# Performance work log

Measured on AMD Instinct MI355X. Metric: run time of the kernel, lower is better.

Reference implementation:

```python
import jax, jax.numpy as jnp
import numpy as np

B, D, H, Wd = 8, 64, 256, 256
EMB = 256
NFEAT = 18
NBINS = 16


def setup_inputs() -> dict:
    key = jax.random.key(0)
    k1, k2 = jax.random.split(key, 2)
    volume = jax.random.normal(k1, (B, D, H, Wd), jnp.float32)
    W = jax.random.normal(k2, (NFEAT, EMB), jnp.float32) * 0.1
    b = jnp.zeros((EMB,), jnp.float32)
    gamma = jnp.ones((EMB,), jnp.float32)
    beta = jnp.zeros((EMB,), jnp.float32)
    return {"volume": volume, "W": W, "b": b, "gamma": gamma, "beta": beta}


def _slice_features(sl):
    # sl: [H, W] single slice; mask derived from 80th percentile threshold
    h, w = sl.shape
    flat = sl.reshape(-1)
    npix = flat.shape[0]
    thresh = jnp.quantile(flat, 0.8)  # torch.quantile default: linear interp
    mask = flat >= thresh
    mf = mask.astype(sl.dtype)
    n = mf.sum()  # >= 1 by construction (max always passes)

    mean = (mf * flat).sum() / n
    c = flat - mean
    std = jnp.sqrt((mf * c * c).sum() / n)  # unbiased=False
    std_eps = jnp.maximum(std, 1e-6)
    skew = jnp.clip(((mf * c**3).sum() / n) / std_eps**3, -50.0, 50.0)
    kurt = jnp.clip(((mf * c**4).sum() / n) / std_eps**4, 0.0, 100.0)
    msq = (mf * flat * flat).sum() / n
    absmean = (mf * jnp.abs(flat)).sum() / n

    # sorted masked values: unmasked pushed to +inf end
    big = jnp.finfo(sl.dtype).max
    vs = jnp.sort(jnp.where(mask, flat, big))
    nm1 = n - 1.0
    last = nm1.astype(jnp.int32)

    def quant(p):
        pos = p * nm1
        lo = jnp.floor(pos)
        fr = pos - lo
        lo_i = lo.astype(jnp.int32)
        hi_i = jnp.minimum(lo_i + 1, last)
        return vs[lo_i] * (1.0 - fr) + vs[hi_i] * fr

    q25, q50, q75 = quant(0.25), quant(0.5), quant(0.75)
    vmin = vs[0]
    vmax = vs[last]

    # 16-bin histogram entropy over masked values (torch.histc semantics)
    rng = vmax - vmin
    denom = jnp.where(rng > 0, rng, 1.0)
    bins = jnp.clip(jnp.floor((flat - vmin) / denom * NBINS).astype(jnp.int32), 0, NBINS - 1)
    hist = jnp.zeros((NBINS,), sl.dtype).at[bins].add(mf)
    probs = jnp.maximum(hist / jnp.maximum(hist.sum(), 1.0), 1e-6)
    ent = jnp.where(jnp.isclose(vmin, vmax), 0.0, -(probs * jnp.log(probs)).sum())

    # numpy-style gradient magnitude (central diff interior, one-sided edges)
    gy, gx = jnp.gradient(sl)
    gm = jnp.sqrt(gy * gy + gx * gx).reshape(-1)
    gm_mean = (mf * gm).sum() / n
    gm_std = jnp.sqrt((mf * (gm - gm_mean) ** 2).sum() / n)

    # normalized centroid of the mask
    yi = (jnp.arange(npix) // w).astype(sl.dtype)
    xi = (jnp.arange(npix) % w).astype(sl.dtype)
    cy = (mf * yi).sum() / n / max(h - 1, 1)
    cx = (mf * xi).sum() / n / max(w - 1, 1)

    frac = n / npix  # mask.float().mean() == mask.sum()/numel
    return jnp.stack([mean, std, vmin, vmax, q25, q50, q75, msq, ent,
                      skew, kurt, frac, gm_mean, gm_std, cy, cx, frac, absmean])


def reference(volume, W, b, gamma, beta):
    bsz, depth, h, w = volume.shape
    feats = jax.vmap(_slice_features)(volume.reshape(bsz * depth, h, w))
    feats = feats.reshape(bsz, depth, NFEAT)
    x = feats @ W + b
    mu = x.mean(-1, keepdims=True)
    var = ((x - mu) ** 2).mean(-1, keepdims=True)
    tokens = (x - mu) / jnp.sqrt(var + 1e-5) * gamma + beta
    padding_mask = jnp.zeros((bsz, depth), dtype=bool)
    return tokens, padding_mask
```

## Files before the change

### kernel.cpp

```cpp
#include <hip/hip_runtime.h>
#include <stdint.h>

#define NPIX     65536
#define NTHREADS 1024
#define NSLICES  512
#define NFEAT    18
#define EMB      256
#define THRESH_RANK 52428u
#define NB       24
#define IVMAX    4
#define EPT4     16

__device__ __forceinline__ uint32_t f2key(float f) {
  uint32_t u = __float_as_uint(f);
  return u ^ ((uint32_t)((int32_t)u >> 31) | 0x80000000u);
}
__device__ __forceinline__ float key2f(uint32_t k) {
  uint32_t u = (k & 0x80000000u) ? (k ^ 0x80000000u) : ~k;
  return __uint_as_float(u);
}

__device__ void scan2048(uint32_t* H, uint32_t* Wsum) {
  int tid = threadIdx.x, lane = tid & 63, wid = tid >> 6;
  uint32_t a1 = H[2 * tid + 1];
  uint32_t v = H[2 * tid] + a1;
  for (int d = 1; d < 64; d <<= 1) {
    uint32_t t = __shfl_up(v, d);
    if (lane >= d) v += t;
  }
  if (lane == 63) Wsum[wid] = v;
  __syncthreads();
  uint32_t woff = 0;
  for (int w = 0; w < wid; ++w) woff += Wsum[w];
  v += woff;
  H[2 * tid + 1] = v;
  H[2 * tid]     = v - a1;
  __syncthreads();
}

__device__ __forceinline__ int wfind2048(const uint32_t* C, uint32_t r, int lane) {
  unsigned long long m = __ballot(C[lane * 32 + 31] > r);
  int chunk = __builtin_ctzll(m);
  unsigned long long m2 = __ballot((lane < 32) && (C[chunk * 32 + lane] > r));
  int off = __builtin_ctzll(m2);
  return chunk * 32 + off;
}
__device__ __forceinline__ int wfind256(const uint32_t* P, uint32_t r, int lane) {
  unsigned long long m = __ballot(P[lane * 4 + 3] > r);
  int chunk = __builtin_ctzll(m);
  int off = 0;
  while (off < 3 && P[chunk * 4 + off] <= r) ++off;
  return chunk * 4 + off;
}
__device__ __forceinline__ void wscan256(uint32_t* H, int lane) {
  uint32_t h0 = H[lane * 4 + 0], h1 = H[lane * 4 + 1];
  uint32_t h2 = H[lane * 4 + 2], h3 = H[lane * 4 + 3];
  uint32_t s = h0 + h1 + h2 + h3, inc = s;
  for (int d = 1; d < 64; d <<= 1) { uint32_t o = __shfl_up(inc, d); if (lane >= d) inc += o; }
  uint32_t base = inc - s;
  H[lane * 4 + 0] = base + h0;
  H[lane * 4 + 1] = base + h0 + h1;
  H[lane * 4 + 2] = base + h0 + h1 + h2;
  H[lane * 4 + 3] = base + s;
}

__device__ __forceinline__ int slotOf(uint32_t b, const uint32_t* ivLo, const uint32_t* ivHi,
                                      const uint32_t* ivS0, int niv) {
  for (int j = 0; j < niv; ++j)
    if (b >= ivLo[j] && b <= ivHi[j]) return (int)(ivS0[j] + b - ivLo[j]);
  return -1;
}

__device__ void plan_from_bins(int m, const uint32_t* pbin,
                               uint32_t* ivLo, uint32_t* ivHi, uint32_t* ivS0,
                               int* pniv, int* pnslots) {
  uint32_t b[6];
  for (int i = 0; i < m; ++i) b[i] = pbin[i];
  for (int i = 1; i < m; ++i) {
    uint32_t x = b[i]; int j = i - 1;
    while (j >= 0 && b[j] > x) { b[j + 1] = b[j]; --j; }
    b[j + 1] = x;
  }
  int niv = 0; uint32_t s0 = 0; int i = 0;
  while (i < m && niv < IVMAX) {
    uint32_t lo = b[i], hi = b[i]; ++i;
    while (i < m && b[i] <= hi + 1) { hi = max(hi, b[i]); ++i; }
    ivLo[niv] = lo; ivHi[niv] = hi; ivS0[niv] = s0;
    s0 += hi - lo + 1; ++niv;
  }
  for (int j = niv; j < IVMAX; ++j) { ivLo[j] = 0xFFFFu; ivHi[j] = 0u; ivS0[j] = 0u; }
  *pniv = niv; *pnslots = (int)s0;
}

__global__ __launch_bounds__(NTHREADS) void feat_kernel(const float* __restrict__ vol,
                                                        float* __restrict__ feats) {
  __shared__ uint32_t HC1[2048];
  __shared__ uint32_t L2H[NB * 256];
  __shared__ uint32_t Wsum[16];
  __shared__ double   tmpD9[16 * 9];
  __shared__ double   s_red[9];
  __shared__ uint32_t H16[16 * 16];
  __shared__ uint32_t smaxkey;
  __shared__ uint32_t s_ivLo[IVMAX], s_ivHi[IVMAX], s_ivS0[IVMAX];
  __shared__ int      s_niv, s_nslots;
  __shared__ float    s_thresh;
  __shared__ uint32_t s_cnlt;
  __shared__ float    s_qA[3], s_qB[3], s_qfr[3];
  __shared__ int      s_qdup[3];
  __shared__ uint32_t s_prank[6], s_pbin[6];
  __shared__ uint8_t  s_ptag[6];
  __shared__ int      s_npend;

  const int tid  = threadIdx.x;
  const int lane = tid & 63;
  const int wid  = tid >> 6;
  const float*  sl  = vol + (size_t)blockIdx.x * NPIX;
  const float4* sl4 = (const float4*)sl;

  HC1[2 * tid] = 0; HC1[2 * tid + 1] = 0;
  if (tid == 0) smaxkey = 0u;
  if (tid < 256) H16[tid] = 0u;
  __syncthreads();
  uint32_t mk = 0u;
#pragma unroll 4
  for (int t = 0; t < EPT4; ++t) {
    float4 f = sl4[tid + t * NTHREADS];
    uint32_t k0 = f2key(f.x), k1 = f2key(f.y), k2 = f2key(f.z), k3 = f2key(f.w);
    mk = max(mk, max(max(k0, k1), max(k2, k3)));
    atomicAdd(&HC1[k0 >> 21], 1u);
    atomicAdd(&HC1[k1 >> 21], 1u);
    atomicAdd(&HC1[k2 >> 21], 1u);
    atomicAdd(&HC1[k3 >> 21], 1u);
  }
  for (int d = 32; d > 0; d >>= 1) { uint32_t o = __shfl_down(mk, d); mk = max(mk, o); }
  if (lane == 0) atomicMax(&smaxkey, mk);
  __syncthreads();
  scan2048(HC1, Wsum);

  if (tid < 64) {
    int b1t = wfind2048(HC1, THRESH_RANK, lane);
    uint32_t clo  = b1t ? HC1[b1t - 1] : 0u;
    uint32_t cmax = min(THRESH_RANK, HC1[b1t] - 1u);
    uint32_t rl[4], rh[4];
    rl[0] = (uint32_t)b1t; rh[0] = (uint32_t)b1t;
    const float pp[3] = {0.25f, 0.5f, 0.75f};
#pragma unroll
    for (int qi = 0; qi < 3; ++qi) {
      float p = pp[qi];
      uint32_t rlo = clo  + (uint32_t)(int)floorf(p * ((float)(NPIX - clo)  - 1.0f));
      uint32_t rhi = cmax + (uint32_t)(int)floorf(p * ((float)(NPIX - cmax) - 1.0f)) + 1u;
      if (rhi > NPIX - 1u) rhi = NPIX - 1u;
      if (rlo > rhi) rlo = rhi;
      uint32_t ba = (uint32_t)wfind2048(HC1, rlo, lane);
      uint32_t bb = (uint32_t)wfind2048(HC1, rhi, lane);
      if (bb > ba + 5u) bb = ba + 5u;
      rl[qi + 1] = ba; rh[qi + 1] = bb;
    }
    if (lane == 0) {
      for (int i = 1; i < 4; ++i) {
        uint32_t xl = rl[i], xh = rh[i]; int j = i - 1;
        while (j >= 0 && rl[j] > xl) { rl[j + 1] = rl[j]; rh[j + 1] = rh[j]; --j; }
        rl[j + 1] = xl; rh[j + 1] = xh;
      }
      int niv = 0; uint32_t s0 = 0; int i = 0;
      while (i < 4 && niv < IVMAX && s0 < NB) {
        uint32_t lo = rl[i], hi = rh[i]; ++i;
        while (i < 4 && rl[i] <= hi + 1u) { hi = max(hi, rh[i]); ++i; }
        uint32_t cnt = hi - lo + 1u;
        if (s0 + cnt > NB) { cnt = NB - s0; hi = lo + cnt - 1u; }
        s_ivLo[niv] = lo; s_ivHi[niv] = hi; s_ivS0[niv] = s0;
        s0 += cnt; ++niv;
      }
      for (int j = niv; j < IVMAX; ++j) { s_ivLo[j] = 0xFFFFu; s_ivHi[j] = 0u; s_ivS0[j] = 0u; }
      s_niv = niv; s_nslots = (int)s0;
    }
  }
  __syncthreads();

  for (int round = 0; round < 4; ++round) {
    {
      int ns = s_nslots;
      for (int i = tid; i < ns * 256; i += NTHREADS) L2H[i] = 0u;
    }
    __syncthreads();
    {
      uint32_t lo0 = s_ivLo[0], hi0 = s_ivHi[0]; int s00 = (int)s_ivS0[0] - (int)lo0;
      uint32_t lo1 = s_ivLo[1], hi1 = s_ivHi[1]; int s01 = (int)s_ivS0[1] - (int)lo1;
      uint32_t lo2 = s_ivLo[2], hi2 = s_ivHi[2]; int s02 = (int)s_ivS0[2] - (int)lo2;
      uint32_t lo3 = s_ivLo[3], hi3 = s_ivHi[3]; int s03 = (int)s_ivS0[3] - (int)lo3;
      float fL0 = key2f(lo0 << 21);
      float fH0 = (hi0 >= 2047u) ? __builtin_inff() : key2f((hi0 + 1u) << 21);
      float fL1 = key2f(lo1 << 21);
      float fH1 = (hi1 >= 2047u) ? __builtin_inff() : key2f((hi1 + 1u) << 21);
      float fL2 = key2f(lo2 << 21);
      float fH2 = (hi2 >= 2047u) ? __builtin_inff() : key2f((hi2 + 1u) << 21);
      float fL3 = key2f(lo3 << 21);
      float fH3 = (hi3 >= 2047u) ? __builtin_inff() : key2f((hi3 + 1u) << 21);
#pragma unroll 4
      for (int t = 0; t < EPT4; ++t) {
        float4 f = sl4[tid + t * NTHREADS];
#define PB(vv)                                                                  \
        { float v_ = (vv);                                                      \
          if (v_ >= fL0) {                                                      \
            int sb = -0x40000000;                                               \
            if      (v_ < fH0)              sb = s00;                           \
            else if (v_ >= fL1 && v_ < fH1) sb = s01;                           \
            else if (v_ >= fL2 && v_ < fH2) sb = s02;                           \
            else if (v_ >= fL3 && v_ < fH3) sb = s03;                           \
            if (sb != -0x40000000) {                                            \
              uint32_t k = f2key(v_);                                           \
              atomicAdd(&L2H[(uint32_t)(sb + (int)(k >> 21)) * 256 + ((k >> 13) & 255u)], 1u); \
            } } }
        PB(f.x) PB(f.y) PB(f.z) PB(f.w)
#undef PB
      }
    }
    __syncthreads();
    {
      int ns = s_nslots;
      for (int s = wid; s < ns; s += 16) wscan256(&L2H[s * 256], lane);
    }
    __syncthreads();

    if (tid < 64) {
      int niv = s_niv;
      if (round == 0) {
        int b1t = wfind2048(HC1, THRESH_RANK, lane);
        uint32_t below = b1t ? HC1[b1t - 1] : 0u;
        int sl_ = slotOf((uint32_t)b1t, s_ivLo, s_ivHi, s_ivS0, niv);
        const uint32_t* P = &L2H[sl_ * 256];
        int b2 = wfind256(P, THRESH_RANK - below, lane);
        uint32_t cnlt = below + (b2 ? P[b2 - 1] : 0u);
        float th = key2f(((uint32_t)b1t << 21) | ((uint32_t)b2 << 13));
        if (lane == 0) { s_thresh = th; s_cnlt = cnlt; }
        uint32_t n = NPIX - cnlt, t0 = cnlt;
        float nm1f = (float)n - 1.0f;
        int last = (int)nm1f;
        const float pp[3] = {0.25f, 0.5f, 0.75f};
        int np = 0;
        for (int qi = 0; qi < 3; ++qi) {
          float pos = pp[qi] * nm1f;
          float lof = floorf(pos);
          float fr = pos - lof;
          int lo_i = (int)lof;
          int hi_i = min(lo_i + 1, last);
          bool needB = (fr > 0.0f) && (hi_i != lo_i);
          if (lane == 0) { s_qfr[qi] = fr; s_qdup[qi] = needB ? 0 : 1; }
          {
            uint32_t r = t0 + (uint32_t)lo_i;
            int b = wfind2048(HC1, r, lane);
            uint32_t bw = b ? HC1[b - 1] : 0u;
            int sq = slotOf((uint32_t)b, s_ivLo, s_ivHi, s_ivS0, niv);
            if (sq >= 0) {
              const uint32_t* Pq = &L2H[sq * 256];
              int b2q = wfind256(Pq, r - bw, lane);
              float v = key2f(((uint32_t)b << 21) | ((uint32_t)b2q << 13));
              if (lane == 0) { s_qA[qi] = v; s_qB[qi] = v; }
            } else {
              if (lane == 0) { s_prank[np] = r; s_ptag[np] = (uint8_t)(qi * 2); s_pbin[np] = (uint32_t)b; }
              ++np;
            }
          }
          if (needB) {
            uint32_t r = t0 + (uint32_t)hi_i;
            int b = wfind2048(HC1, r, lane);
            uint32_t bw = b ? HC1[b - 1] : 0u;
            int sq = slotOf((uint32_t)b, s_ivLo, s_ivHi, s_ivS0, niv);
            if (sq >= 0) {
              const uint32_t* Pq = &L2H[sq * 256];
              int b2q = wfind256(Pq, r - bw, lane);
              float v = key2f(((uint32_t)b << 21) | ((uint32_t)b2q << 13));
              if (lane == 0) s_qB[qi] = v;
            } else {
              if (lane == 0) { s_prank[np] = r; s_ptag[np] = (uint8_t)(qi * 2 + 1); s_pbin[np] = (uint32_t)b; }
              ++np;
            }
          }
        }
        if (lane == 0) {
          s_npend = np;
          if (np > 0) plan_from_bins(np, s_pbin, s_ivLo, s_ivHi, s_ivS0, &s_niv, &s_nslots);
        }
      } else {
        int np = s_npend, newnp = 0;
        for (int i = 0; i < np; ++i) {
          uint32_t r = s_prank[i];
          int tg = s_ptag[i];
          int b = wfind2048(HC1, r, lane);
          uint32_t bw = b ? HC1[b - 1] : 0u;
          int sq = slotOf((uint32_t)b, s_ivLo, s_ivHi, s_ivS0, niv);
          if (sq >= 0) {
            const uint32_t* Pq = &L2H[sq * 256];
            int b2q = wfind256(Pq, r - bw, lane);
            float v = key2f(((uint32_t)b << 21) | ((uint32_t)b2q << 13));
            if (lane == 0) { if (tg & 1) s_qB[tg >> 1] = v; else s_qA[tg >> 1] = v; }
          } else {
            if (lane == 0) { s_prank[newnp] = r; s_ptag[newnp] = (uint8_t)tg; s_pbin[newnp] = (uint32_t)b; }
            ++newnp;
          }
        }
        if (lane == 0) {
          s_npend = newnp;
          if (newnp > 0) plan_from_bins(newnp, s_pbin, s_ivLo, s_ivHi, s_ivS0, &s_niv, &s_nslots);
        }
      }
    }
    __syncthreads();
    if (s_npend == 0) break;
    __syncthreads();
  }

  const float thresh = s_thresh;
  const uint32_t n = NPIX - s_cnlt;
  const float vmax  = key2f(smaxkey);
  const float vminf = thresh;

  float rng = vmax - vminf;
  float denomf = (rng > 0.0f) ? rng : 1.0f;
  float sc16 = 16.0f / denomf;
  float sxl = 0, sx2l = 0, sx3l = 0, sx4l = 0, sabl = 0, sgl = 0, sg2l = 0;
  uint32_t syi = 0, sxi = 0;
#pragma unroll 4
  for (int t = 0; t < EPT4; ++t) {
    int i4 = tid + t * NTHREADS;
    float4 v = sl4[i4];
    float lf = __shfl_up(v.w, 1);
    float rt = __shfl_down(v.x, 1);
    bool m0 = v.x >= thresh, m1 = v.y >= thresh, m2 = v.z >= thresh, m3 = v.w >= thresh;
    if (m0 | m1 | m2 | m3) {
      int y = i4 >> 6;
      float4 up = sl4[(y > 0)   ? (i4 - 64) : i4];
      float4 dn = sl4[(y < 255) ? (i4 + 64) : i4];
      float gy0, gy1, gy2, gy3;
      if (y == 0)        { gy0 = dn.x - v.x; gy1 = dn.y - v.y; gy2 = dn.z - v.z; gy3 = dn.w - v.w; }
      else if (y == 255) { gy0 = v.x - up.x; gy1 = v.y - up.y; gy2 = v.z - up.z; gy3 = v.w - up.w; }
      else { gy0 = 0.5f * (dn.x - up.x); gy1 = 0.5f * (dn.y - up.y);
             gy2 = 0.5f * (dn.z - up.z); gy3 = 0.5f * (dn.w - up.w); }
      float gx0 = (lane == 0)  ? (v.y - v.x) : 0.5f * (v.y - lf);
      float gx1 = 0.5f * (v.z - v.x);
      float gx2 = 0.5f * (v.w - v.y);
      float gx3 = (lane == 63) ? (v.w - v.z) : 0.5f * (rt - v.z);
#define DOC(mc, vc, gyc, gxc, xc)                                              \
      if (mc) {                                                                \
        float gm = sqrtf((gyc) * (gyc) + (gxc) * (gxc));                       \
        sgl += gm; sg2l += gm * gm;                                            \
        float v2 = (vc) * (vc);                                                \
        sxl += (vc); sx2l += v2; sx3l += v2 * (vc); sx4l += v2 * v2;           \
        sabl += fabsf(vc);                                                     \
        syi += (uint32_t)y; sxi += (uint32_t)((lane << 2) + (xc));             \
        float bf = floorf(((vc) - vminf) * sc16);                              \
        int bin = (int)bf; bin = bin < 0 ? 0 : (bin > 15 ? 15 : bin);          \
        atomicAdd(&H16[(wid << 4) + bin], 1u);                                 \
      }
      DOC(m0, v.x, gy0, gx0, 0)
      DOC(m1, v.y, gy1, gx1, 1)
      DOC(m2, v.z, gy2, gx2, 2)
      DOC(m3, v.w, gy3, gx3, 3)
#undef DOC
    }
  }

  {
    float af[7] = {sxl, sx2l, sx3l, sx4l, sabl, sgl, sg2l};
#pragma unroll
    for (int k = 0; k < 7; ++k)
      for (int d = 32; d > 0; d >>= 1) af[k] += __shfl_down(af[k], d);
    uint32_t au0 = syi, au1 = sxi;
    for (int d = 32; d > 0; d >>= 1) { au0 += __shfl_down(au0, d); au1 += __shfl_down(au1, d); }
    if (lane == 0) {
#pragma unroll
      for (int k = 0; k < 7; ++k) tmpD9[wid * 9 + k] = (double)af[k];
      tmpD9[wid * 9 + 7] = (double)au0;
      tmpD9[wid * 9 + 8] = (double)au1;
    }
  }
  __syncthreads();
  if (tid < 64) {
    double r0 = 0, r1 = 0, r2 = 0, r3 = 0, r4 = 0, r5 = 0, r6 = 0, r7 = 0, r8 = 0;
    if (lane < 16) {
      r0 = tmpD9[lane * 9 + 0]; r1 = tmpD9[lane * 9 + 1]; r2 = tmpD9[lane * 9 + 2];
      r3 = tmpD9[lane * 9 + 3]; r4 = tmpD9[lane * 9 + 4]; r5 = tmpD9[lane * 9 + 5];
      r6 = tmpD9[lane * 9 + 6]; r7 = tmpD9[lane * 9 + 7]; r8 = tmpD9[lane * 9 + 8];
    }
    for (int d = 8; d > 0; d >>= 1) {
      r0 += __shfl_down(r0, d); r1 += __shfl_down(r1, d); r2 += __shfl_down(r2, d);
      r3 += __shfl_down(r3, d); r4 += __shfl_down(r4, d); r5 += __shfl_down(r5, d);
      r6 += __shfl_down(r6, d); r7 += __shfl_down(r7, d); r8 += __shfl_down(r8, d);
    }
    if (lane == 0) {
      s_red[0] = r0; s_red[1] = r1; s_red[2] = r2; s_red[3] = r3; s_red[4] = r4;
      s_red[5] = r5; s_red[6] = r6; s_red[7] = r7; s_red[8] = r8;
    }
  }
  __syncthreads();

  if (tid == 0) {
    double sx = s_red[0], sx2 = s_red[1], sx3 = s_red[2], sx4 = s_red[3];
    double sab = s_red[4], sg = s_red[5], sg2 = s_red[6], syid = s_red[7], sxid = s_red[8];
    double dn = (double)n;
    double mean = sx / dn;
    double M2 = sx2 - sx * sx / dn;
    double std_ = sqrt(M2 / dn);
    double se = fmax(std_, 1e-6);
    double S3 = sx3 - 3.0 * mean * sx2 + 2.0 * dn * mean * mean * mean;
    double S4 = sx4 - 4.0 * mean * sx3 + 6.0 * mean * mean * sx2
                - 3.0 * dn * mean * mean * mean * mean;
    double skew = (S3 / dn) / (se * se * se);
    skew = fmin(fmax(skew, -50.0), 50.0);
    double kurt = (S4 / dn) / (se * se * se * se);
    kurt = fmin(fmax(kurt, 0.0), 100.0);
    double msq = sx2 / dn;
    double absmean = sab / dn;

    double ent = 0.0;
    double nden = fmax(dn, 1.0);
    for (int bi = 0; bi < 16; ++bi) {
      uint32_t hb = 0;
#pragma unroll
      for (int w = 0; w < 16; ++w) hb += H16[(w << 4) + bi];
      double p = fmax((double)hb / nden, 1e-6);
      ent -= p * log(p);
    }
    if (fabsf(vminf - vmax) <= 1e-8f + 1e-5f * fabsf(vmax)) ent = 0.0;

    double gmean = sg / dn;
    double gstd = sqrt(fmax(sg2 / dn - gmean * gmean, 0.0));
    double cy = (syid / dn) / 255.0;
    double cx = (sxid / dn) / 255.0;
    double frac = dn / (double)NPIX;

    float qv[3];
#pragma unroll
    for (int qi = 0; qi < 3; ++qi) {
      float A = s_qA[qi];
      float Bv = s_qdup[qi] ? A : s_qB[qi];
      float fr = s_qfr[qi];
      qv[qi] = A * (1.0f - fr) + Bv * fr;
    }

    float* fo = feats + (size_t)blockIdx.x * NFEAT;
    fo[0]  = (float)mean;  fo[1]  = (float)std_;  fo[2]  = vminf;       fo[3]  = vmax;
    fo[4]  = qv[0];        fo[5]  = qv[1];        fo[6]  = qv[2];       fo[7]  = (float)msq;
    fo[8]  = (float)ent;   fo[9]  = (float)skew;  fo[10] = (float)kurt; fo[11] = (float)frac;
    fo[12] = (float)gmean; fo[13] = (float)gstd;  fo[14] = (float)cy;   fo[15] = (float)cx;
    fo[16] = (float)frac;  fo[17] = (float)absmean;
  }
}

__global__ __launch_bounds__(EMB) void token_kernel(const float* __restrict__ feats,
                                                    const float* __restrict__ W,
                                                    const float* __restrict__ b,
                                                    const float* __restrict__ gamma,
                                                    const float* __restrict__ beta,
                                                    float* __restrict__ out,
                                                    float* __restrict__ maskout) {
  __shared__ float f[NFEAT];
  __shared__ float red[4];
  int s = blockIdx.x, e = threadIdx.x;
  if (e < NFEAT) f[e] = feats[(size_t)s * NFEAT + e];
  __syncthreads();
  float acc = b[e];
#pragma unroll
  for (int k = 0; k < NFEAT; ++k) acc += f[k] * W[k * EMB + e];
  int lane = e & 63, wd = e >> 6;
  float sum = acc;
  for (int d = 32; d > 0; d >>= 1) sum += __shfl_down(sum, d);
  if (lane == 0) red[wd] = sum;
  __syncthreads();
  float mu = (red[0] + red[1] + red[2] + red[3]) * (1.0f / EMB);
  float c = acc - mu;
  float s2 = c * c;
  for (int d = 32; d > 0; d >>= 1) s2 += __shfl_down(s2, d);
  __syncthreads();
  if (lane == 0) red[wd] = s2;
  __syncthreads();
  float var = (red[0] + red[1] + red[2] + red[3]) * (1.0f / EMB);
  float o = c / sqrtf(var + 1e-5f) * gamma[e] + beta[e];
  out[(size_t)s * EMB + e] = o;
  if (e == 0) maskout[s] = 0.0f;
}

extern "C" void kernel_launch(void* const* d_in, const int* in_sizes, int n_in,
                              void* d_out, int out_size, void* d_ws, size_t ws_size,
                              hipStream_t stream) {
  const float* vol   = (const float*)d_in[0];
  const float* W     = (const float*)d_in[1];
  const float* b     = (const float*)d_in[2];
  const float* gamma = (const float*)d_in[3];
  const float* beta  = (const float*)d_in[4];
  float* out = (float*)d_out;
  float* feats = (float*)d_ws;

  feat_kernel<<<NSLICES, NTHREADS, 0, stream>>>(vol, feats);
  token_kernel<<<NSLICES, EMB, 0, stream>>>(feats, W, b, gamma, beta,
                                            out, out + (size_t)NSLICES * EMB);
}
```

Baseline: 96.30 us.

## Plan refinement bins from a pixel sample and fuse token projection into feature kernel

Builds a coarse histogram from an 8192-pixel sample to predict which coarse bins hold the threshold and quantiles. The full coarse histogram and the first refined histogram are then computed in one pass over the slice instead of two. If the prediction misses, extra refinement rounds act as a fallback, with the round limit raised to five. The separate token kernel is also folded into the feature kernel, which removes a launch and the feats round trip. The cost is a sample-dependent extra pass when the guess is wrong and 768 idle threads during the token epilogue.

```diff
diff --git a/kernel.cpp b/kernel.cpp
--- a/kernel.cpp
+++ b/kernel.cpp
@@ -7,6 +7,8 @@
 #define NFEAT    18
 #define EMB      256
 #define THRESH_RANK 52428u
+#define SAMP_RANK   6553u
+#define NSAMP    8192u
 #define NB       24
 #define IVMAX    4
 #define EPT4     16
@@ -92,8 +94,11 @@
   *pniv = niv; *pnslots = (int)s0;
 }
 
-__global__ __launch_bounds__(NTHREADS) void feat_kernel(const float* __restrict__ vol,
-                                                        float* __restrict__ feats) {
+__global__ __launch_bounds__(NTHREADS) void feat_token_kernel(
+    const float* __restrict__ vol, const float* __restrict__ Wm,
+    const float* __restrict__ bvec, const float* __restrict__ gammav,
+    const float* __restrict__ betav, float* __restrict__ out,
+    float* __restrict__ maskout) {
   __shared__ uint32_t HC1[2048];
   __shared__ uint32_t L2H[NB * 256];
   __shared__ uint32_t Wsum[16];
@@ -109,7 +114,9 @@
   __shared__ int      s_qdup[3];
   __shared__ uint32_t s_prank[6], s_pbin[6];
   __shared__ uint8_t  s_ptag[6];
-  __shared__ int      s_npend;
+  __shared__ int      s_npend, s_have_thr;
+  __shared__ float    s_feat[NFEAT];
+  __shared__ float    red4[4];
 
   const int tid  = threadIdx.x;
   const int lane = tid & 63;
@@ -117,55 +124,61 @@
   const float*  sl  = vol + (size_t)blockIdx.x * NPIX;
   const float4* sl4 = (const float4*)sl;
 
-  HC1[2 * tid] = 0; HC1[2 * tid + 1] = 0;
-  if (tid == 0) smaxkey = 0u;
+  L2H[2 * tid] = 0u; L2H[2 * tid + 1] = 0u;
+  if (tid == 0) { smaxkey = 0u; s_have_thr = 0; s_npend = 0; }
   if (tid < 256) H16[tid] = 0u;
   __syncthreads();
-  uint32_t mk = 0u;
-#pragma unroll 4
-  for (int t = 0; t < EPT4; ++t) {
-    float4 f = sl4[tid + t * NTHREADS];
-    uint32_t k0 = f2key(f.x), k1 = f2key(f.y), k2 = f2key(f.z), k3 = f2key(f.w);
-    mk = max(mk, max(max(k0, k1), max(k2, k3)));
-    atomicAdd(&HC1[k0 >> 21], 1u);
-    atomicAdd(&HC1[k1 >> 21], 1u);
-    atomicAdd(&HC1[k2 >> 21], 1u);
-    atomicAdd(&HC1[k3 >> 21], 1u);
-  }
-  for (int d = 32; d > 0; d >>= 1) { uint32_t o = __shfl_down(mk, d); mk = max(mk, o); }
-  if (lane == 0) atomicMax(&smaxkey, mk);
-  __syncthreads();
-  scan2048(HC1, Wsum);
+
+  {
+    int j0 = tid, j1 = tid + NTHREADS;
+    float4 a = sl4[((j0 >> 6) << 9) | (j0 & 63)];
+    float4 c = sl4[((j1 >> 6) << 9) | (j1 & 63)];
+    atomicAdd(&L2H[f2key(a.x) >> 21], 1u);
+    atomicAdd(&L2H[f2key(a.y) >> 21], 1u);
+    atomicAdd(&L2H[f2key(a.z) >> 21], 1u);
+    atomicAdd(&L2H[f2key(a.w) >> 21], 1u);
+    atomicAdd(&L2H[f2key(c.x) >> 21], 1u);
+    atomicAdd(&L2H[f2key(c.y) >> 21], 1u);
+    atomicAdd(&L2H[f2key(c.z) >> 21], 1u);
+    atomicAdd(&L2H[f2key(c.w) >> 21], 1u);
+  }
+  __syncthreads();
+  scan2048(L2H, Wsum);
 
   if (tid < 64) {
-    int b1t = wfind2048(HC1, THRESH_RANK, lane);
-    uint32_t clo  = b1t ? HC1[b1t - 1] : 0u;
-    uint32_t cmax = min(THRESH_RANK, HC1[b1t] - 1u);
-    uint32_t rl[4], rh[4];
-    rl[0] = (uint32_t)b1t; rh[0] = (uint32_t)b1t;
+    const uint32_t* SH = L2H;
+    int b1t = wfind2048(SH, SAMP_RANK, lane);
+    uint32_t clo  = b1t ? SH[b1t - 1] : 0u;
+    uint32_t cmax = min(SAMP_RANK, SH[b1t] - 1u);
+    int rl[4], rh[4];
+    rl[0] = b1t - 1; rh[0] = b1t + 1;
     const float pp[3] = {0.25f, 0.5f, 0.75f};
 #pragma unroll
     for (int qi = 0; qi < 3; ++qi) {
       float p = pp[qi];
-      uint32_t rlo = clo  + (uint32_t)(int)floorf(p * ((float)(NPIX - clo)  - 1.0f));
-      uint32_t rhi = cmax + (uint32_t)(int)floorf(p * ((float)(NPIX - cmax) - 1.0f)) + 1u;
-      if (rhi > NPIX - 1u) rhi = NPIX - 1u;
+      uint32_t rlo = clo  + (uint32_t)(int)floorf(p * ((float)(NSAMP - clo)  - 1.0f));
+      uint32_t rhi = cmax + (uint32_t)(int)floorf(p * ((float)(NSAMP - cmax) - 1.0f)) + 1u;
+      if (rhi > NSAMP - 1u) rhi = NSAMP - 1u;
       if (rlo > rhi) rlo = rhi;
-      uint32_t ba = (uint32_t)wfind2048(HC1, rlo, lane);
-      uint32_t bb = (uint32_t)wfind2048(HC1, rhi, lane);
-      if (bb > ba + 5u) bb = ba + 5u;
-      rl[qi + 1] = ba; rh[qi + 1] = bb;
+      int ba = wfind2048(SH, rlo, lane);
+      int bb = wfind2048(SH, rhi, lane);
+      rl[qi + 1] = ba - 1; rh[qi + 1] = bb + 1;
     }
     if (lane == 0) {
+#pragma unroll
+      for (int i = 0; i < 4; ++i) {
+        if (rl[i] < 0) rl[i] = 0;
+        if (rh[i] > 2047) rh[i] = 2047;
+      }
       for (int i = 1; i < 4; ++i) {
-        uint32_t xl = rl[i], xh = rh[i]; int j = i - 1;
+        int xl = rl[i], xh = rh[i]; int j = i - 1;
         while (j >= 0 && rl[j] > xl) { rl[j + 1] = rl[j]; rh[j + 1] = rh[j]; --j; }
         rl[j + 1] = xl; rh[j + 1] = xh;
       }
       int niv = 0; uint32_t s0 = 0; int i = 0;
-      while (i < 4 && niv < IVMAX && s0 < NB) {
-        uint32_t lo = rl[i], hi = rh[i]; ++i;
-        while (i < 4 && rl[i] <= hi + 1u) { hi = max(hi, rh[i]); ++i; }
+      while (i < 4 && niv < IVMAX && (int)s0 < NB) {
+        uint32_t lo = (uint32_t)rl[i], hi = (uint32_t)rh[i]; ++i;
+        while (i < 4 && (uint32_t)rl[i] <= hi + 1u) { hi = max(hi, (uint32_t)rh[i]); ++i; }
         uint32_t cnt = hi - lo + 1u;
         if (s0 + cnt > NB) { cnt = NB - s0; hi = lo + cnt - 1u; }
         s_ivLo[niv] = lo; s_ivHi[niv] = hi; s_ivS0[niv] = s0;
@@ -177,109 +190,157 @@
   }
   __syncthreads();
 
-  for (int round = 0; round < 4; ++round) {
-    {
-      int ns = s_nslots;
-      for (int i = tid; i < ns * 256; i += NTHREADS) L2H[i] = 0u;
-    }
-    __syncthreads();
-    {
-      uint32_t lo0 = s_ivLo[0], hi0 = s_ivHi[0]; int s00 = (int)s_ivS0[0] - (int)lo0;
-      uint32_t lo1 = s_ivLo[1], hi1 = s_ivHi[1]; int s01 = (int)s_ivS0[1] - (int)lo1;
-      uint32_t lo2 = s_ivLo[2], hi2 = s_ivHi[2]; int s02 = (int)s_ivS0[2] - (int)lo2;
-      uint32_t lo3 = s_ivLo[3], hi3 = s_ivHi[3]; int s03 = (int)s_ivS0[3] - (int)lo3;
-      float fL0 = key2f(lo0 << 21);
-      float fH0 = (hi0 >= 2047u) ? __builtin_inff() : key2f((hi0 + 1u) << 21);
-      float fL1 = key2f(lo1 << 21);
-      float fH1 = (hi1 >= 2047u) ? __builtin_inff() : key2f((hi1 + 1u) << 21);
-      float fL2 = key2f(lo2 << 21);
-      float fH2 = (hi2 >= 2047u) ? __builtin_inff() : key2f((hi2 + 1u) << 21);
-      float fL3 = key2f(lo3 << 21);
-      float fH3 = (hi3 >= 2047u) ? __builtin_inff() : key2f((hi3 + 1u) << 21);
+  HC1[2 * tid] = 0u; HC1[2 * tid + 1] = 0u;
+  { int ns = s_nslots; for (int i = tid; i < ns * 256; i += NTHREADS) L2H[i] = 0u; }
+  __syncthreads();
+
+  {
+    uint32_t lo0 = s_ivLo[0], hi0 = s_ivHi[0]; int s00 = (int)s_ivS0[0] - (int)lo0;
+    uint32_t lo1 = s_ivLo[1], hi1 = s_ivHi[1]; int s01 = (int)s_ivS0[1] - (int)lo1;
+    uint32_t lo2 = s_ivLo[2], hi2 = s_ivHi[2]; int s02 = (int)s_ivS0[2] - (int)lo2;
+    uint32_t lo3 = s_ivLo[3], hi3 = s_ivHi[3]; int s03 = (int)s_ivS0[3] - (int)lo3;
+    float fL0 = key2f(lo0 << 21);
+    float fH0 = (hi0 >= 2047u) ? __builtin_inff() : key2f((hi0 + 1u) << 21);
+    float fL1 = key2f(lo1 << 21);
+    float fH1 = (hi1 >= 2047u) ? __builtin_inff() : key2f((hi1 + 1u) << 21);
+    float fL2 = key2f(lo2 << 21);
+    float fH2 = (hi2 >= 2047u) ? __builtin_inff() : key2f((hi2 + 1u) << 21);
+    float fL3 = key2f(lo3 << 21);
+    float fH3 = (hi3 >= 2047u) ? __builtin_inff() : key2f((hi3 + 1u) << 21);
+    uint32_t mk = 0u;
 #pragma unroll 4
-      for (int t = 0; t < EPT4; ++t) {
-        float4 f = sl4[tid + t * NTHREADS];
+    for (int t = 0; t < EPT4; ++t) {
+      float4 f = sl4[tid + t * NTHREADS];
+#define FUSED(vv)                                                               \
+      { float v_ = (vv); uint32_t k = f2key(v_);                                \
+        mk = max(mk, k);                                                        \
+        atomicAdd(&HC1[k >> 21], 1u);                                           \
+        if (v_ >= fL0) {                                                        \
+          int sb = -0x40000000;                                                 \
+          if      (v_ < fH0)              sb = s00;                             \
+          else if (v_ >= fL1 && v_ < fH1) sb = s01;                             \
+          else if (v_ >= fL2 && v_ < fH2) sb = s02;                             \
+          else if (v_ >= fL3 && v_ < fH3) sb = s03;                             \
+          if (sb != -0x40000000)                                                \
+            atomicAdd(&L2H[(uint32_t)(sb + (int)(k >> 21)) * 256 + ((k >> 13) & 255u)], 1u); \
+        } }
+      FUSED(f.x) FUSED(f.y) FUSED(f.z) FUSED(f.w)
+#undef FUSED
+    }
+    for (int d = 32; d > 0; d >>= 1) { uint32_t o = __shfl_down(mk, d); mk = max(mk, o); }
+    if (lane == 0) atomicMax(&smaxkey, mk);
+  }
+  __syncthreads();
+  scan2048(HC1, Wsum);
+  { int ns = s_nslots; for (int s = wid; s < ns; s += 16) wscan256(&L2H[s * 256], lane); }
+  __syncthreads();
+
+  for (int round = 0; round < 5; ++round) {
+    if (round > 0) {
+      { int ns = s_nslots; for (int i = tid; i < ns * 256; i += NTHREADS) L2H[i] = 0u; }
+      __syncthreads();
+      {
+        uint32_t lo0 = s_ivLo[0], hi0 = s_ivHi[0]; int s00 = (int)s_ivS0[0] - (int)lo0;
+        uint32_t lo1 = s_ivLo[1], hi1 = s_ivHi[1]; int s01 = (int)s_ivS0[1] - (int)lo1;
+        uint32_t lo2 = s_ivLo[2], hi2 = s_ivHi[2]; int s02 = (int)s_ivS0[2] - (int)lo2;
+        uint32_t lo3 = s_ivLo[3], hi3 = s_ivHi[3]; int s03 = (int)s_ivS0[3] - (int)lo3;
+        float fL0 = key2f(lo0 << 21);
+        float fH0 = (hi0 >= 2047u) ? __builtin_inff() : key2f((hi0 + 1u) << 21);
+        float fL1 = key2f(lo1 << 21);
+        float fH1 = (hi1 >= 2047u) ? __builtin_inff() : key2f((hi1 + 1u) << 21);
+        float fL2 = key2f(lo2 << 21);
+        float fH2 = (hi2 >= 2047u) ? __builtin_inff() : key2f((hi2 + 1u) << 21);
+        float fL3 = key2f(lo3 << 21);
+        float fH3 = (hi3 >= 2047u) ? __builtin_inff() : key2f((hi3 + 1u) << 21);
+#pragma unroll 4
+        for (int t = 0; t < EPT4; ++t) {
+          float4 f = sl4[tid + t * NTHREADS];
 #define PB(vv)                                                                  \
-        { float v_ = (vv);                                                      \
-          if (v_ >= fL0) {                                                      \
-            int sb = -0x40000000;                                               \
-            if      (v_ < fH0)              sb = s00;                           \
-            else if (v_ >= fL1 && v_ < fH1) sb = s01;                           \
-            else if (v_ >= fL2 && v_ < fH2) sb = s02;                           \
-            else if (v_ >= fL3 && v_ < fH3) sb = s03;                           \
-            if (sb != -0x40000000) {                                            \
-              uint32_t k = f2key(v_);                                           \
-              atomicAdd(&L2H[(uint32_t)(sb + (int)(k >> 21)) * 256 + ((k >> 13) & 255u)], 1u); \
-            } } }
-        PB(f.x) PB(f.y) PB(f.z) PB(f.w)
+          { float v_ = (vv);                                                    \
+            if (v_ >= fL0) {                                                    \
+              int sb = -0x40000000;                                             \
+              if      (v_ < fH0)              sb = s00;                         \
+              else if (v_ >= fL1 && v_ < fH1) sb = s01;                         \
+              else if (v_ >= fL2 && v_ < fH2) sb = s02;                         \
+              else if (v_ >= fL3 && v_ < fH3) sb = s03;                         \
+              if (sb != -0x40000000) {                                          \
+                uint32_t k = f2key(v_);                                         \
+                atomicAdd(&L2H[(uint32_t)(sb + (int)(k >> 21)) * 256 + ((k >> 13) & 255u)], 1u); \
+              } } }
+          PB(f.x) PB(f.y) PB(f.z) PB(f.w)
 #undef PB
+        }
       }
-    }
-    __syncthreads();
-    {
-      int ns = s_nslots;
-      for (int s = wid; s < ns; s += 16) wscan256(&L2H[s * 256], lane);
-    }
-    __syncthreads();
+      __syncthreads();
+      { int ns = s_nslots; for (int s = wid; s < ns; s += 16) wscan256(&L2H[s * 256], lane); }
+      __syncthreads();
+    }
 
     if (tid < 64) {
       int niv = s_niv;
-      if (round == 0) {
+      if (!s_have_thr) {
         int b1t = wfind2048(HC1, THRESH_RANK, lane);
         uint32_t below = b1t ? HC1[b1t - 1] : 0u;
-        int sl_ = slotOf((uint32_t)b1t, s_ivLo, s_ivHi, s_ivS0, niv);
-        const uint32_t* P = &L2H[sl_ * 256];
-        int b2 = wfind256(P, THRESH_RANK - below, lane);
-        uint32_t cnlt = below + (b2 ? P[b2 - 1] : 0u);
-        float th = key2f(((uint32_t)b1t << 21) | ((uint32_t)b2 << 13));
-        if (lane == 0) { s_thresh = th; s_cnlt = cnlt; }
-        uint32_t n = NPIX - cnlt, t0 = cnlt;
-        float nm1f = (float)n - 1.0f;
-        int last = (int)nm1f;
-        const float pp[3] = {0.25f, 0.5f, 0.75f};
-        int np = 0;
-        for (int qi = 0; qi < 3; ++qi) {
-          float pos = pp[qi] * nm1f;
-          float lof = floorf(pos);
-          float fr = pos - lof;
-          int lo_i = (int)lof;
-          int hi_i = min(lo_i + 1, last);
-          bool needB = (fr > 0.0f) && (hi_i != lo_i);
-          if (lane == 0) { s_qfr[qi] = fr; s_qdup[qi] = needB ? 0 : 1; }
-          {
-            uint32_t r = t0 + (uint32_t)lo_i;
-            int b = wfind2048(HC1, r, lane);
-            uint32_t bw = b ? HC1[b - 1] : 0u;
-            int sq = slotOf((uint32_t)b, s_ivLo, s_ivHi, s_ivS0, niv);
-            if (sq >= 0) {
-              const uint32_t* Pq = &L2H[sq * 256];
-              int b2q = wfind256(Pq, r - bw, lane);
-              float v = key2f(((uint32_t)b << 21) | ((uint32_t)b2q << 13));
-              if (lane == 0) { s_qA[qi] = v; s_qB[qi] = v; }
-            } else {
-              if (lane == 0) { s_prank[np] = r; s_ptag[np] = (uint8_t)(qi * 2); s_pbin[np] = (uint32_t)b; }
-              ++np;
+        int sq = slotOf((uint32_t)b1t, s_ivLo, s_ivHi, s_ivS0, niv);
+        if (sq >= 0) {
+          const uint32_t* P = &L2H[sq * 256];
+          int b2 = wfind256(P, THRESH_RANK - below, lane);
+          uint32_t cnlt = below + (b2 ? P[b2 - 1] : 0u);
+          float th = key2f(((uint32_t)b1t << 21) | ((uint32_t)b2 << 13));
+          if (lane == 0) { s_thresh = th; s_cnlt = cnlt; s_have_thr = 1; }
+          uint32_t n = NPIX - cnlt, t0 = cnlt;
+          float nm1f = (float)n - 1.0f;
+          int last = (int)nm1f;
+          const float pp[3] = {0.25f, 0.5f, 0.75f};
+          int np = 0;
+          for (int qi = 0; qi < 3; ++qi) {
+            float pos = pp[qi] * nm1f;
+            float lof = floorf(pos);
+            float fr = pos - lof;
+            int lo_i = (int)lof;
+            int hi_i = min(lo_i + 1, last);
+            bool needB = (fr > 0.0f) && (hi_i != lo_i);
+            if (lane == 0) { s_qfr[qi] = fr; s_qdup[qi] = needB ? 0 : 1; }
+            {
+              uint32_t r = t0 + (uint32_t)lo_i;
+              int b = wfind2048(HC1, r, lane);
+              uint32_t bw = b ? HC1[b - 1] : 0u;
+              int sq2 = slotOf((uint32_t)b, s_ivLo, s_ivHi, s_ivS0, niv);
+              if (sq2 >= 0) {
+                const uint32_t* Pq = &L2H[sq2 * 256];
+                int b2q = wfind256(Pq, r - bw, lane);
+                float v = key2f(((uint32_t)b << 21) | ((uint32_t)b2q << 13));
+                if (lane == 0) { s_qA[qi] = v; s_qB[qi] = v; }
+              } else {
+                if (lane == 0) { s_prank[np] = r; s_ptag[np] = (uint8_t)(qi * 2); s_pbin[np] = (uint32_t)b; }
+                ++np;
+              }
+            }
+            if (needB) {
+              uint32_t r = t0 + (uint32_t)hi_i;
+              int b = wfind2048(HC1, r, lane);
+              uint32_t bw = b ? HC1[b - 1] : 0u;
+              int sq2 = slotOf((uint32_t)b, s_ivLo, s_ivHi, s_ivS0, niv);
+              if (sq2 >= 0) {
+                const uint32_t* Pq = &L2H[sq2 * 256];
+                int b2q = wfind256(Pq, r - bw, lane);
+                float v = key2f(((uint32_t)b << 21) | ((uint32_t)b2q << 13));
+                if (lane == 0) s_qB[qi] = v;
+              } else {
+                if (lane == 0) { s_prank[np] = r; s_ptag[np] = (uint8_t)(qi * 2 + 1); s_pbin[np] = (uint32_t)b; }
+                ++np;
+              }
             }
           }
-          if (needB) {
-            uint32_t r = t0 + (uint32_t)hi_i;
-            int b = wfind2048(HC1, r, lane);
-            uint32_t bw = b ? HC1[b - 1] : 0u;
-            int sq = slotOf((uint32_t)b, s_ivLo, s_ivHi, s_ivS0, niv);
-            if (sq >= 0) {
-              const uint32_t* Pq = &L2H[sq * 256];
-              int b2q = wfind256(Pq, r - bw, lane);
-              float v = key2f(((uint32_t)b << 21) | ((uint32_t)b2q << 13));
-              if (lane == 0) s_qB[qi] = v;
-            } else {
-              if (lane == 0) { s_prank[np] = r; s_ptag[np] = (uint8_t)(qi * 2 + 1); s_pbin[np] = (uint32_t)b; }
-              ++np;
-            }
+          if (lane == 0) {
+            s_npend = np;
+            if (np > 0) plan_from_bins(np, s_pbin, s_ivLo, s_ivHi, s_ivS0, &s_niv, &s_nslots);
           }
-        }
-        if (lane == 0) {
-          s_npend = np;
-          if (np > 0) plan_from_bins(np, s_pbin, s_ivLo, s_ivHi, s_ivS0, &s_niv, &s_nslots);
+        } else {
+          if (lane == 0) {
+            s_pbin[0] = (uint32_t)b1t; s_npend = 1;
+            plan_from_bins(1, s_pbin, s_ivLo, s_ivHi, s_ivS0, &s_niv, &s_nslots);
+          }
         }
       } else {
         int np = s_npend, newnp = 0;
@@ -438,46 +499,38 @@
       qv[qi] = A * (1.0f - fr) + Bv * fr;
     }
 
-    float* fo = feats + (size_t)blockIdx.x * NFEAT;
-    fo[0]  = (float)mean;  fo[1]  = (float)std_;  fo[2]  = vminf;       fo[3]  = vmax;
-    fo[4]  = qv[0];        fo[5]  = qv[1];        fo[6]  = qv[2];       fo[7]  = (float)msq;
-    fo[8]  = (float)ent;   fo[9]  = (float)skew;  fo[10] = (float)kurt; fo[11] = (float)frac;
-    fo[12] = (float)gmean; fo[13] = (float)gstd;  fo[14] = (float)cy;   fo[15] = (float)cx;
-    fo[16] = (float)frac;  fo[17] = (float)absmean;
-  }
-}
-
-__global__ __launch_bounds__(EMB) void token_kernel(const float* __restrict__ feats,
-                                                    const float* __restrict__ W,
-                                                    const float* __restrict__ b,
-                                                    const float* __restrict__ gamma,
-                                                    const float* __restrict__ beta,
-                                                    float* __restrict__ out,
-                                                    float* __restrict__ maskout) {
-  __shared__ float f[NFEAT];
-  __shared__ float red[4];
-  int s = blockIdx.x, e = threadIdx.x;
-  if (e < NFEAT) f[e] = feats[(size_t)s * NFEAT + e];
-  __syncthreads();
-  float acc = b[e];
-#pragma unroll
-  for (int k = 0; k < NFEAT; ++k) acc += f[k] * W[k * EMB + e];
-  int lane = e & 63, wd = e >> 6;
+    s_feat[0]  = (float)mean;  s_feat[1]  = (float)std_;  s_feat[2]  = vminf;
+    s_feat[3]  = vmax;         s_feat[4]  = qv[0];        s_feat[5]  = qv[1];
+    s_feat[6]  = qv[2];        s_feat[7]  = (float)msq;   s_feat[8]  = (float)ent;
+    s_feat[9]  = (float)skew;  s_feat[10] = (float)kurt;  s_feat[11] = (float)frac;
+    s_feat[12] = (float)gmean; s_feat[13] = (float)gstd;  s_feat[14] = (float)cy;
+    s_feat[15] = (float)cx;    s_feat[16] = (float)frac;  s_feat[17] = (float)absmean;
+  }
+  __syncthreads();
+
+  float acc = 0.0f;
+  if (tid < EMB) {
+    acc = bvec[tid];
+#pragma unroll
+    for (int k = 0; k < NFEAT; ++k) acc += s_feat[k] * Wm[k * EMB + tid];
+  }
   float sum = acc;
   for (int d = 32; d > 0; d >>= 1) sum += __shfl_down(sum, d);
-  if (lane == 0) red[wd] = sum;
-  __syncthreads();
-  float mu = (red[0] + red[1] + red[2] + red[3]) * (1.0f / EMB);
+  if (tid < EMB && lane == 0) red4[wid] = sum;
+  __syncthreads();
+  float mu = (red4[0] + red4[1] + red4[2] + red4[3]) * (1.0f / EMB);
   float c = acc - mu;
   float s2 = c * c;
   for (int d = 32; d > 0; d >>= 1) s2 += __shfl_down(s2, d);
   __syncthreads();
-  if (lane == 0) red[wd] = s2;
-  __syncthreads();
-  float var = (red[0] + red[1] + red[2] + red[3]) * (1.0f / EMB);
-  float o = c / sqrtf(var + 1e-5f) * gamma[e] + beta[e];
-  out[(size_t)s * EMB + e] = o;
-  if (e == 0) maskout[s] = 0.0f;
+  if (tid < EMB && lane == 0) red4[wid] = s2;
+  __syncthreads();
+  if (tid < EMB) {
+    float var = (red4[0] + red4[1] + red4[2] + red4[3]) * (1.0f / EMB);
+    float o = c / sqrtf(var + 1e-5f) * gammav[tid] + betav[tid];
+    out[(size_t)blockIdx.x * EMB + tid] = o;
+  }
+  if (tid == 0) maskout[blockIdx.x] = 0.0f;
 }
 
 extern "C" void kernel_launch(void* const* d_in, const int* in_sizes, int n_in,
@@ -489,9 +542,7 @@
   const float* gamma = (const float*)d_in[3];
   const float* beta  = (const float*)d_in[4];
   float* out = (float*)d_out;
-  float* feats = (float*)d_ws;
-
-  feat_kernel<<<NSLICES, NTHREADS, 0, stream>>>(vol, feats);
-  token_kernel<<<NSLICES, EMB, 0, stream>>>(feats, W, b, gamma, beta,
-                                            out, out + (size_t)NSLICES * EMB);
-}
+
+  feat_token_kernel<<<NSLICES, NTHREADS, 0, stream>>>(
+      vol, W, b, gamma, beta, out, out + (size_t)NSLICES * EMB);
+}
```

New measurement: 110.8 us. +15.1%, slower.
